# Optimization experiments

Measured on AMD Instinct MI355X. Metric: run time of the kernel, lower is better.

## Reference

```python
import jax, jax.numpy as jnp
import numpy as np

NEG_INF = -1e5  # module default neg_inf


def setup_inputs() -> dict:
    key = jax.random.key(0)
    k1, k2 = jax.random.split(key)
    B, T, V, U = 64, 1000, 512, 256
    log_posteriors = jax.random.normal(k1, (B, T, V), dtype=jnp.float32)
    lens = jnp.ones((B,), dtype=jnp.float32)
    phns = jax.random.randint(k2, (B, U), 0, V)
    phn_lens = jnp.ones((B,), dtype=jnp.float32)
    return {"log_posteriors": log_posteriors, "lens": lens, "phns": phns, "phn_lens": phn_lens}


def _forward_scores(log_posteriors, lens, phns, phn_lens):
    B, T, V = log_posteriors.shape
    U = phns.shape[1]
    lens_abs = jnp.round(lens * T).astype(jnp.int32)
    phn_lens_abs = jnp.round(phn_lens * U).astype(jnp.int32)

    # --- pi: all initial mass on first phoneme ---
    pi = jnp.full((B, U), NEG_INF, dtype=jnp.float32).at[:, 0].set(0.0)

    # --- transition log-probs: self-loop + advance-by-one, length-masked, row log_softmax ---
    base = jnp.eye(U, dtype=jnp.float32) + jnp.eye(U, k=1, dtype=jnp.float32)  # (U,U)
    m = jnp.arange(U)[None, :] < phn_lens_abs[:, None]  # (B,U) valid-phoneme mask
    m2 = m[:, :, None] & m[:, None, :]  # (B,U,U)
    masked = base[None, :, :] * m2.astype(jnp.float32)
    logits = jnp.where(masked == 1.0, 1.0, -jnp.inf)
    trans = jax.nn.log_softmax(logits, axis=2)
    # nan (all -inf rows) and -inf -> neg_inf, as in the torch module
    trans = jnp.where(jnp.isnan(trans) | jnp.isinf(trans), NEG_INF, trans)  # (B,U,U)

    # --- emissions rearranged to phoneme-sequence order: (B, U, T) as (T, B, U) scan seq ---
    mask_t = jnp.arange(T)[None, :] < lens_abs[:, None]  # (B,T)
    ep = jnp.where(mask_t[:, :, None], log_posteriors, NEG_INF)
    idx = jnp.broadcast_to(phns[:, None, :], (B, T, U))
    gathered = jnp.take_along_axis(ep, idx, axis=2)  # (B,T,U)
    emiss = jnp.where(m[:, None, :], gathered, NEG_INF)  # (B,T,U)
    emiss_seq = jnp.swapaxes(emiss, 0, 1)  # (T,B,U)

    # --- forward DP: alpha[t,i] = logsumexp_j(trans[j,i] + alpha[t-1,j]) + emiss[t,i] ---
    transT = jnp.swapaxes(trans, 1, 2)  # (B, to, from)
    alpha0 = pi + emiss_seq[0]  # (B,U), unmasked as in torch (masked entries ~2*neg_inf anyway)

    def step(alpha, e_t):
        x = jax.nn.logsumexp(transT + alpha[:, None, :], axis=2)  # batch_log_matvecmul
        alpha_new = jnp.where(m, x + e_t, NEG_INF)
        return alpha_new, None

    alphaT, _ = jax.lax.scan(step, alpha0, emiss_seq[1:])
    return jax.nn.logsumexp(alphaT, axis=1)  # (B,) log-likelihoods


def reference(log_posteriors, lens, phns, phn_lens):
    return _forward_scores(log_posteriors, lens, phns, phn_lens)
```

## Files before the change

### kernel.cpp

```cpp
#include <hip/hip_runtime.h>
#include <math.h>

constexpr int Bc = 64;
constexpr int Tc = 1000;
constexpr int Vc = 512;
constexpr int Uc = 256;
constexpr int CH = 50;
constexpr int NCH = Tc / CH;
constexpr int PW = 7;
constexpr int SLOTS = 4;

constexpr int GW = 2;
constexpr int GNR = 10;
constexpr int GROWS = GW * GNR;
constexpr int GBLK = Tc / GROWS;

#define NEG_INF_F (-100000.0f)
#define LOG2E_F 1.44269504088896340736f
#define LN2_F 0.69314718055994530942f
#define DEAD_F (-1.0e9f)

__device__ __forceinline__ float fexp2(float x) {
#if __has_builtin(__builtin_amdgcn_exp2f)
    return __builtin_amdgcn_exp2f(x);
#else
    return __expf(x * LN2_F);
#endif
}
__device__ __forceinline__ float flog2(float x) {
#if __has_builtin(__builtin_amdgcn_logf)
    return __builtin_amdgcn_logf(x);
#else
    return __logf(x) * LOG2E_F;
#endif
}

__device__ __forceinline__ float l2add(float x, float y) {
    float m = fmaxf(x, y);
    float p = fexp2(-fabsf(x - y));
    return m + flog2(1.0f + p);
}

__device__ __forceinline__ float waveshr1(float x, float lane0val) {
    return __int_as_float(__builtin_amdgcn_update_dpp(
        __float_as_int(lane0val), __float_as_int(x),
        0x138 , 0xF, 0xF, false));
}

__device__ __forceinline__ double waveshr1_f64(double x) {
    int lo = __double2loint(x), hi = __double2hiint(x);
    int slo = __builtin_amdgcn_update_dpp(0, lo, 0x138, 0xF, 0xF, false);
    int shi = __builtin_amdgcn_update_dpp(0, hi, 0x138, 0xF, 0xF, false);
    return __hiloint2double(shi, slo);
}

__device__ __forceinline__ void hmm_step_f64(double rr[4], const float4 ev) {
    double nb0 = waveshr1_f64(rr[3]);
    double s0 = rr[0] + nb0;
    double s1 = rr[1] + rr[0];
    double s2 = rr[2] + rr[1];
    double s3 = rr[3] + rr[2];
    rr[0] = s0 * (double)ev.x;
    rr[1] = s1 * (double)ev.y;
    rr[2] = s2 * (double)ev.z;
    rr[3] = s3 * (double)ev.w;
}

__device__ __forceinline__ void hmm_step(float rr[4], const float4 ev) {
    float nb0 = waveshr1(rr[3], DEAD_F);
    float e[4] = {ev.x, ev.y, ev.z, ev.w};
    float nb[4] = {nb0, rr[0], rr[1], rr[2]};
#pragma unroll
    for (int c = 0; c < 4; ++c) {
        float x = rr[c], y = nb[c];
        float m = fmaxf(x, y);
        float p = fexp2(-fabsf(x - y));
        float me = m + e[c];
        rr[c] = me + flog2(1.0f + p);
    }
}

__device__ __forceinline__ void dma16(const float* gsrc, float* lds, int lane) {
    typedef const __attribute__((address_space(1))) unsigned int* gp_t;
    typedef __attribute__((address_space(3))) unsigned int* lp_t;
    __builtin_amdgcn_global_load_lds((gp_t)(const void*)(gsrc + 4 * lane),
                                     (lp_t)(void*)lds, 16, 0, 0);
}

__global__ __launch_bounds__(128, 2) void gather_kernel(
    const float* __restrict__ lp, const float* __restrict__ lens,
    const int* __restrict__ phns, const float* __restrict__ phn_lens,
    float* __restrict__ el) {
    __shared__ float stage[GW][GNR][Vc];
    const int b = blockIdx.x;
    const int t0 = blockIdx.y * GROWS;
    const int tid = threadIdx.x;
    const int wave = tid >> 6;
    const int lane = tid & 63;
    const int Tv = (int)rintf(lens[b] * (float)Tc);
    const int Uv = (int)rintf(phn_lens[b] * (float)Uc);
    const float* lpb = lp + (size_t)b * Tc * Vc;
    float* elb = el + ((size_t)b * Tc + t0) * Uc;

    int col[4];
    float off[4];
    bool pv[4];
    int4 cc = *(const int4*)(phns + (size_t)b * Uc + 4 * lane);
    int c4[4] = {cc.x, cc.y, cc.z, cc.w};
#pragma unroll
    for (int c = 0; c < 4; ++c) {
        int v = c4[c];
        v = v < 0 ? 0 : (v > Vc - 1 ? Vc - 1 : v);
        col[c] = v;
        int i = 4 * lane + c;
        pv[c] = (i < Uv);
        off[c] = (i == Uv - 1) ? 0.0f : -1.0f;
    }

    float* stw = &stage[wave][0][0];
#pragma unroll
    for (int j = 0; j < GNR; ++j) {
        int r = wave + j * GW;
        const float* gsrc = lpb + (size_t)(t0 + r) * Vc;
        float* st = stw + j * Vc;
        dma16(gsrc, st, lane);
        dma16(gsrc + 256, st + 256, lane);
    }

    auto do_rows = [&](int j0) {
#pragma unroll
        for (int j = j0; j < j0 + GNR / 2; ++j) {
            int r = wave + j * GW;
            const bool tv = (t0 + r) < Tv;
            const float* st = stw + j * Vc;
            float ev[4];
#pragma unroll
            for (int c = 0; c < 4; ++c) {
                float e = st[col[c]];
                ev[c] = (pv[c] && tv) ? fexp2(fmaf(e, LOG2E_F, off[c])) : 0.0f;
            }
            *(float4*)(elb + (size_t)r * Uc + 4 * lane) =
                make_float4(ev[0], ev[1], ev[2], ev[3]);
        }
    };

    __builtin_amdgcn_s_waitcnt(0x0f7A);
    do_rows(0);
    __builtin_amdgcn_s_waitcnt(0x0f70);
    do_rows(GNR / 2);
}

__global__ __launch_bounds__(64, 1) void scan_kernel(
    const float* __restrict__ el, const float* __restrict__ phn_lens,
    float* __restrict__ out) {
    __shared__ float ebuf[2][CH][Uc];
    const int b = blockIdx.x;
    const int lane = threadIdx.x & 63;
    const int Uv = (int)rintf(phn_lens[b] * (float)Uc);
    const float* eb = el + (size_t)b * Tc * Uc;
    double rr[4];
    float S = 0.0f;

    auto fill = [&](int k) {
        const float* src = eb + (size_t)k * CH * Uc;
        float* dst = &ebuf[k & 1][0][0];
#pragma unroll 5
        for (int r = 0; r < CH; ++r)
            dma16(src + (size_t)r * Uc, dst + r * Uc, lane);
    };

    auto consume = [&](int k) {
        const float4* base = (const float4*)&ebuf[k & 1][0][0] + lane;
        int r = 0;
        if (k == 0) {
            float4 e0 = base[0];
            float ea[4] = {e0.x, e0.y, e0.z, e0.w};
#pragma unroll
            for (int c = 0; c < 4; ++c)
                rr[c] = (4 * lane + c == 0) ? (double)ea[c] : 0.0;
            r = 1;
        }
        float4 q0, q1, q2, q3;
        if (r + 0 < CH) q0 = base[(r + 0) * 64];
        if (r + 1 < CH) q1 = base[(r + 1) * 64];
        if (r + 2 < CH) q2 = base[(r + 2) * 64];
        if (r + 3 < CH) q3 = base[(r + 3) * 64];
        while (r + 4 <= CH) {
            float4 e0 = q0, e1 = q1, e2v = q2, e3 = q3;
            if (r + 4 < CH) q0 = base[(r + 4) * 64];
            if (r + 5 < CH) q1 = base[(r + 5) * 64];
            if (r + 6 < CH) q2 = base[(r + 6) * 64];
            if (r + 7 < CH) q3 = base[(r + 7) * 64];
            hmm_step_f64(rr, e0);
            hmm_step_f64(rr, e1);
            hmm_step_f64(rr, e2v);
            hmm_step_f64(rr, e3);
            r += 4;
        }
        if (r + 0 < CH) hmm_step_f64(rr, q0);
        if (r + 1 < CH) hmm_step_f64(rr, q1);
        if (r + 2 < CH) hmm_step_f64(rr, q2);
    };

    fill(0);
    __builtin_amdgcn_s_waitcnt(0x0f70);
    for (int k = 0; k < NCH; ++k) {
        if (k + 1 < NCH) fill(k + 1);
        consume(k);
        double m = fmax(fmax(rr[0], rr[1]), fmax(rr[2], rr[3]));
#pragma unroll
        for (int o = 32; o >= 1; o >>= 1) m = fmax(m, __shfl_xor(m, o, 64));
        if (m > 0.0) {
            int ik = ((__double2hiint(m) >> 20) & 0x7ff) - 1023;
            S += (float)ik;
            const double sc = __hiloint2double((1023 - ik) << 20, 0);
            rr[0] *= sc; rr[1] *= sc; rr[2] *= sc; rr[3] *= sc;
        }
        __builtin_amdgcn_s_waitcnt(0x0f70);
    }

    double a = 0.0;
#pragma unroll
    for (int c = 0; c < 4; ++c)
        a += rr[c] * ((4 * lane + c == Uv - 1) ? 1.0 : 2.0);
#pragma unroll
    for (int o = 32; o >= 1; o >>= 1) a += __shfl_xor(a, o, 64);
    if (lane == 0) out[b] = (flog2((float)a) + S) * LN2_F;
}

__global__ __launch_bounds__(512, 1) void fused_hmm_kernel(
    const float* __restrict__ lp, const float* __restrict__ lens,
    const int* __restrict__ phns, const float* __restrict__ phn_lens,
    float* __restrict__ out) {
    __shared__ float ebuf[2][CH][Uc];
    __shared__ float stage[PW][SLOTS][Vc];
    const int b = blockIdx.x;
    const int tid = threadIdx.x;
    const int wave = tid >> 6;
    const int lane = tid & 63;
    const int Tv = (int)rintf(lens[b] * (float)Tc);
    const int Uv = (int)rintf(phn_lens[b] * (float)Uc);
    const float* lpb = lp + (size_t)b * Tc * Vc;

    int col[4];
    float off[4];
    bool pv[4];
    float rr[4];

    if (wave > 0) {
        int4 cc = *(const int4*)(phns + (size_t)b * Uc + 4 * lane);
        int c4[4] = {cc.x, cc.y, cc.z, cc.w};
#pragma unroll
        for (int c = 0; c < 4; ++c) {
            int v = c4[c];
            v = v < 0 ? 0 : (v > Vc - 1 ? Vc - 1 : v);
            col[c] = v;
            int i = 4 * lane + c;
            pv[c] = (i < Uv);
            off[c] = (i == Uv - 1) ? 0.0f : -1.0f;
        }
    }

    auto fill = [&](int k) {
        float* dst = &ebuf[k & 1][0][0];
        const int tb = k * CH;
        const int r0 = wave - 1;
        float* stw = &stage[wave - 1][0][0];
#pragma unroll
        for (int half = 0; half < 2; ++half) {
#pragma unroll
            for (int jj = 0; jj < SLOTS; ++jj) {
                int r = r0 + (half * SLOTS + jj) * PW;
                if (r < CH) {
                    const float* gsrc = lpb + (size_t)(tb + r) * Vc;
                    float* st = stw + jj * Vc;
                    dma16(gsrc, st, lane);
                    dma16(gsrc + 256, st + 256, lane);
                }
            }
            __builtin_amdgcn_s_waitcnt(0x0f70);
#pragma unroll
            for (int jj = 0; jj < SLOTS; ++jj) {
                int r = r0 + (half * SLOTS + jj) * PW;
                if (r < CH) {
                    const bool tv = (tb + r) < Tv;
                    const float* st = stw + jj * Vc;
                    float ev[4];
#pragma unroll
                    for (int c = 0; c < 4; ++c) {
                        float e = st[col[c]];
                        ev[c] = (pv[c] && tv) ? fmaf(e, LOG2E_F, off[c])
                                              : (NEG_INF_F * LOG2E_F + off[c]);
                    }
                    *(float4*)(dst + r * Uc + 4 * lane) =
                        make_float4(ev[0], ev[1], ev[2], ev[3]);
                }
            }
        }
    };

    auto consume = [&](int k) {
        const float4* base = (const float4*)&ebuf[k & 1][0][0] + lane;
        int r = 0;
        if (k == 0) {
            float4 e0 = base[0];
            float ea[4] = {e0.x, e0.y, e0.z, e0.w};
#pragma unroll
            for (int c = 0; c < 4; ++c)
                rr[c] = ((4 * lane + c == 0) ? 0.0f : DEAD_F) + ea[c];
            r = 1;
        }
        float4 q0, q1, q2, q3;
        if (r + 0 < CH) q0 = base[(r + 0) * 64];
        if (r + 1 < CH) q1 = base[(r + 1) * 64];
        if (r + 2 < CH) q2 = base[(r + 2) * 64];
        if (r + 3 < CH) q3 = base[(r + 3) * 64];
        while (r + 4 <= CH) {
            float4 e0 = q0, e1 = q1, e2 = q2, e3 = q3;
            if (r + 4 < CH) q0 = base[(r + 4) * 64];
            if (r + 5 < CH) q1 = base[(r + 5) * 64];
            if (r + 6 < CH) q2 = base[(r + 6) * 64];
            if (r + 7 < CH) q3 = base[(r + 7) * 64];
            hmm_step(rr, e0);
            hmm_step(rr, e1);
            hmm_step(rr, e2);
            hmm_step(rr, e3);
            r += 4;
        }
        if (r + 0 < CH) hmm_step(rr, q0);
        if (r + 1 < CH) hmm_step(rr, q1);
        if (r + 2 < CH) hmm_step(rr, q2);
    };

    if (wave > 0) fill(0);
    __syncthreads();
    for (int k = 0; k < NCH; ++k) {
        if (wave > 0) {
            if (k + 1 < NCH) fill(k + 1);
        } else {
            consume(k);
        }
        __syncthreads();
    }

    if (wave == 0) {
        float a[4];
#pragma unroll
        for (int c = 0; c < 4; ++c)
            a[c] = rr[c] + ((4 * lane + c == Uv - 1) ? 0.0f : 1.0f);
        float r2 = l2add(l2add(a[0], a[1]), l2add(a[2], a[3]));
#pragma unroll
        for (int o = 32; o >= 1; o >>= 1) {
            float t = __shfl_xor(r2, o, 64);
            r2 = l2add(r2, t);
        }
        if (lane == 0) out[b] = r2 * LN2_F;
    }
}

extern "C" void kernel_launch(void* const* d_in, const int* in_sizes, int n_in,
                              void* d_out, int out_size, void* d_ws, size_t ws_size,
                              hipStream_t stream) {
    const float* lp = (const float*)d_in[0];
    const float* lens = (const float*)d_in[1];
    const int* phns = (const int*)d_in[2];
    const float* phn_lens = (const float*)d_in[3];
    float* out = (float*)d_out;
    (void)in_sizes; (void)n_in; (void)out_size;

    const size_t need = (size_t)Bc * Tc * Uc * sizeof(float);
    if (d_ws != nullptr && ws_size >= need) {
        float* el = (float*)d_ws;
        gather_kernel<<<dim3(Bc, GBLK), 128, 0, stream>>>(lp, lens, phns,
                                                          phn_lens, el);
        scan_kernel<<<Bc, 64, 0, stream>>>(el, phn_lens, out);
    } else {
        fused_hmm_kernel<<<Bc, 512, 0, stream>>>(lp, lens, phns, phn_lens, out);
    }
}
```

Baseline: 280.6 us.

## Switch scan recurrence from fp64 to fp32 with per-lane exponent renormalization

The linear-domain forward recurrence in the scan kernel moves from double to float. Each lane now keeps its own exponent offset and renormalizes every four steps. The neighbor value shifted in from the previous lane is rescaled by the exponent difference, and the final reduction uses a log-add across lanes. This removes slow fp64 arithmetic and the per-chunk wave-wide max reduction, at the cost of extra DPP shifts and integer exponent bookkeeping, plus a risk of underflow or precision loss in fp32.

Measured after the change: 277.1 us. No clear change (-1.3%).

```diff
diff --git a/kernel.cpp b/kernel.cpp
--- a/kernel.cpp
+++ b/kernel.cpp
@@ -19,6 +19,7 @@
 #define LOG2E_F 1.44269504088896340736f
 #define LN2_F 0.69314718055994530942f
 #define DEAD_F (-1.0e9f)
+#define EBIAS 30
 
 __device__ __forceinline__ float fexp2(float x) {
 #if __has_builtin(__builtin_amdgcn_exp2f)
@@ -46,24 +47,21 @@
         __float_as_int(lane0val), __float_as_int(x),
         0x138 , 0xF, 0xF, false));
 }
-
-__device__ __forceinline__ double waveshr1_f64(double x) {
-    int lo = __double2loint(x), hi = __double2hiint(x);
-    int slo = __builtin_amdgcn_update_dpp(0, lo, 0x138, 0xF, 0xF, false);
-    int shi = __builtin_amdgcn_update_dpp(0, hi, 0x138, 0xF, 0xF, false);
-    return __hiloint2double(shi, slo);
-}
-
-__device__ __forceinline__ void hmm_step_f64(double rr[4], const float4 ev) {
-    double nb0 = waveshr1_f64(rr[3]);
-    double s0 = rr[0] + nb0;
-    double s1 = rr[1] + rr[0];
-    double s2 = rr[2] + rr[1];
-    double s3 = rr[3] + rr[2];
-    rr[0] = s0 * (double)ev.x;
-    rr[1] = s1 * (double)ev.y;
-    rr[2] = s2 * (double)ev.z;
-    rr[3] = s3 * (double)ev.w;
+__device__ __forceinline__ int waveshr1_i(int x) {
+    return __builtin_amdgcn_update_dpp(x, x, 0x138, 0xF, 0xF, false);
+}
+
+__device__ __forceinline__ void hmm_step_f32(float rr[4], const float4 ev,
+                                             float sc_d) {
+    float nb0 = waveshr1(rr[3], 0.0f) * sc_d;
+    float s0 = rr[0] + nb0;
+    float s1 = rr[1] + rr[0];
+    float s2 = rr[2] + rr[1];
+    float s3 = rr[3] + rr[2];
+    rr[0] = s0 * ev.x;
+    rr[1] = s1 * ev.y;
+    rr[2] = s2 * ev.z;
+    rr[3] = s3 * ev.w;
 }
 
 __device__ __forceinline__ void hmm_step(float rr[4], const float4 ev) {
@@ -158,8 +156,9 @@
     const int lane = threadIdx.x & 63;
     const int Uv = (int)rintf(phn_lens[b] * (float)Uc);
     const float* eb = el + (size_t)b * Tc * Uc;
-    double rr[4];
-    float S = 0.0f;
+    float rr[4];
+    int e = 0;
+    float sc_d = 1.0f;
 
     auto fill = [&](int k) {
         const float* src = eb + (size_t)k * CH * Uc;
@@ -169,6 +168,22 @@
             dma16(src + (size_t)r * Uc, dst + r * Uc, lane);
     };
 
+    auto renorm = [&]() {
+        float m = fmaxf(fmaxf(rr[0], rr[1]), fmaxf(rr[2], rr[3]));
+        int ep_old = waveshr1_i(e);
+        bool nz = (m > 0.0f);
+        int ik = ((__float_as_int(m) >> 23) & 255) - 127 - EBIAS;
+        ik = ik < -96 ? -96 : (ik > 96 ? 96 : ik);
+        const float sc = __int_as_float((127 - ik) << 23);
+        rr[0] *= sc; rr[1] *= sc; rr[2] *= sc; rr[3] *= sc;
+        e = nz ? (e + ik) : ep_old;
+        int ep = waveshr1_i(e);
+        int d = ep - e;
+        int dc = d < -126 ? -126 : (d > 127 ? 127 : d);
+        float sd = __int_as_float((127 + dc) << 23);
+        sc_d = (d < -126) ? 0.0f : sd;
+    };
+
     auto consume = [&](int k) {
         const float4* base = (const float4*)&ebuf[k & 1][0][0] + lane;
         int r = 0;
@@ -177,7 +192,7 @@
             float ea[4] = {e0.x, e0.y, e0.z, e0.w};
 #pragma unroll
             for (int c = 0; c < 4; ++c)
-                rr[c] = (4 * lane + c == 0) ? (double)ea[c] : 0.0;
+                rr[c] = (4 * lane + c == 0) ? ea[c] : 0.0f;
             r = 1;
         }
         float4 q0, q1, q2, q3;
@@ -191,15 +206,18 @@
             if (r + 5 < CH) q1 = base[(r + 5) * 64];
             if (r + 6 < CH) q2 = base[(r + 6) * 64];
             if (r + 7 < CH) q3 = base[(r + 7) * 64];
-            hmm_step_f64(rr, e0);
-            hmm_step_f64(rr, e1);
-            hmm_step_f64(rr, e2v);
-            hmm_step_f64(rr, e3);
+            hmm_step_f32(rr, e0, sc_d);
+            hmm_step_f32(rr, e1, sc_d);
+            hmm_step_f32(rr, e2v, sc_d);
+            hmm_step_f32(rr, e3, sc_d);
+            renorm();
             r += 4;
         }
-        if (r + 0 < CH) hmm_step_f64(rr, q0);
-        if (r + 1 < CH) hmm_step_f64(rr, q1);
-        if (r + 2 < CH) hmm_step_f64(rr, q2);
+        bool tail = false;
+        if (r + 0 < CH) { hmm_step_f32(rr, q0, sc_d); tail = true; }
+        if (r + 1 < CH) { hmm_step_f32(rr, q1, sc_d); }
+        if (r + 2 < CH) { hmm_step_f32(rr, q2, sc_d); }
+        if (tail) renorm();
     };
 
     fill(0);
@@ -207,25 +225,20 @@
     for (int k = 0; k < NCH; ++k) {
         if (k + 1 < NCH) fill(k + 1);
         consume(k);
-        double m = fmax(fmax(rr[0], rr[1]), fmax(rr[2], rr[3]));
-#pragma unroll
-        for (int o = 32; o >= 1; o >>= 1) m = fmax(m, __shfl_xor(m, o, 64));
-        if (m > 0.0) {
-            int ik = ((__double2hiint(m) >> 20) & 0x7ff) - 1023;
-            S += (float)ik;
-            const double sc = __hiloint2double((1023 - ik) << 20, 0);
-            rr[0] *= sc; rr[1] *= sc; rr[2] *= sc; rr[3] *= sc;
-        }
         __builtin_amdgcn_s_waitcnt(0x0f70);
     }
 
-    double a = 0.0;
+    float a = 0.0f;
 #pragma unroll
     for (int c = 0; c < 4; ++c)
-        a += rr[c] * ((4 * lane + c == Uv - 1) ? 1.0 : 2.0);
-#pragma unroll
-    for (int o = 32; o >= 1; o >>= 1) a += __shfl_xor(a, o, 64);
-    if (lane == 0) out[b] = (flog2((float)a) + S) * LN2_F;
+        a += rr[c] * ((4 * lane + c == Uv - 1) ? 1.0f : 2.0f);
+    float v = (a > 0.0f) ? (flog2(a) + (float)e) : -1.0e30f;
+#pragma unroll
+    for (int o = 32; o >= 1; o >>= 1) {
+        float t = __shfl_xor(v, o, 64);
+        v = l2add(v, t);
+    }
+    if (lane == 0) out[b] = v * LN2_F;
 }
 
 __global__ __launch_bounds__(512, 1) void fused_hmm_kernel(
```
